# Performance work log

Measured on AMD Instinct MI355X. Metric: run time of the kernel, lower is better.

The kernel has to match this reference:

```python
import jax, jax.numpy as jnp
import numpy as np

INF = 1000000000000.0
B, H, EMB = 64, 512, 512
V = 32000
S_ENC, S_SEQ = 512, 512
ENC2 = 512  # 2 * encoder_hidden_dim
NUM_OOV = 50


def setup_inputs() -> dict:
    key = jax.random.key(0)
    ks = jax.random.split(key, 24)
    s = 0.02
    nrm = lambda k, shp: jax.random.normal(k, shp, jnp.float32) * s
    inp = {}
    inp["input_ids"] = jax.random.randint(ks[0], (B,), 0, V)
    inp["prev_context"] = jax.random.normal(ks[1], (B, H), jnp.float32)
    inp["h0"] = jax.random.normal(ks[2], (1, B, H), jnp.float32)
    inp["c0"] = jax.random.normal(ks[3], (1, B, H), jnp.float32)
    inp["encoder_outputs"] = jax.random.normal(ks[4], (B, S_ENC, H), jnp.float32)
    inp["seqs_encoding"] = jax.random.normal(ks[5], (B, S_SEQ, ENC2), jnp.float32)
    inp["seqs_encoding_mask"] = jax.random.randint(ks[6], (B, S_SEQ), 0, 2).astype(bool)
    ext = jax.random.randint(ks[7], (B, S_SEQ), 0, V + NUM_OOV)
    inp["ext_idx"] = ext.at[0, 0].set(V + NUM_OOV - 1)  # pin max so num_oov=NUM_OOV
    # parameters (torch Linear convention: y = x @ W.T + b)
    inp["embed"] = nrm(ks[8], (V, EMB))
    inp["W_reduce"] = nrm(ks[9], (EMB, EMB + H)); inp["b_reduce"] = jnp.zeros((EMB,), jnp.float32)
    inp["W_key"] = nrm(ks[10], (H, H)); inp["b_key"] = jnp.zeros((H,), jnp.float32)
    inp["W_comb"] = nrm(ks[11], (H, 2 * H)); inp["b_comb"] = jnp.zeros((H,), jnp.float32)
    inp["W_seqkey"] = nrm(ks[12], (H, ENC2))
    inp["W_ih"] = nrm(ks[13], (4 * H, EMB)); inp["W_hh"] = nrm(ks[14], (4 * H, H))
    inp["b_ih"] = jnp.zeros((4 * H,), jnp.float32); inp["b_hh"] = jnp.zeros((4 * H,), jnp.float32)
    inp["W_out"] = nrm(ks[15], (V, H)); inp["b_out"] = jnp.zeros((V,), jnp.float32)
    return inp


def reference(input_ids, prev_context, h0, c0, encoder_outputs, seqs_encoding,
              seqs_encoding_mask, ext_idx, embed, W_reduce, b_reduce, W_key, b_key,
              W_comb, b_comb, W_seqkey, W_ih, W_hh, b_ih, b_hh, W_out, b_out):
    # embed + (dropout is identity at p=0 / eval) + reduce
    embedded = embed[input_ids]                                   # [B, EMB]
    x = jnp.concatenate([embedded, prev_context], axis=1) @ W_reduce.T + b_reduce  # [B, EMB]
    # single-step, single-layer LSTM (PyTorch gate order i, f, g, o)
    h, c = h0[0], c0[0]
    gates = x @ W_ih.T + b_ih + h @ W_hh.T + b_hh                 # [B, 4H]
    i, f, g, o = jnp.split(gates, 4, axis=-1)
    c1 = jax.nn.sigmoid(f) * c + jax.nn.sigmoid(i) * jnp.tanh(g)
    h1 = jax.nn.sigmoid(o) * jnp.tanh(c1)                         # [B, H]
    output = h1
    # masked attention over encoder_outputs
    enc_mask = encoder_outputs.sum(axis=-1) == 0                  # [B, S_enc]
    keys = encoder_outputs @ W_key.T + b_key                      # [B, S_enc, H]
    energies = jnp.einsum('bsh,bh->bs', keys, output)
    energies = jnp.where(enc_mask, 1e-12, energies)
    attn_weights = jax.nn.softmax(energies, axis=-1)
    context = jnp.einsum('bs,bsh->bh', attn_weights, encoder_outputs)  # [B, H]
    combined = jnp.tanh(jnp.concatenate([output, context], axis=1) @ W_comb.T + b_comb)
    logits = combined @ W_out.T + b_out                           # [B, V]
    # masked attention energies over token sequence for the copy mechanism
    seq_keys = jnp.tanh(seqs_encoding @ W_seqkey.T)               # [B, S_seq, H]
    seq_energies = jnp.einsum('bsh,bh->bs', seq_keys, output)
    seq_energies = jnp.where(seqs_encoding_mask, 1e-12, seq_energies)
    # extended vocab + scatter_max pointer-copy
    extended = jnp.concatenate([logits, jnp.zeros((B, NUM_OOV), logits.dtype)], axis=1)  # [B, V+OOV]
    copy = jnp.full_like(extended, -INF)
    copy = copy.at[jnp.arange(B)[:, None], ext_idx].max(seq_energies)
    copy = jnp.where(copy == -INF, 0.0, copy)
    out = extended + copy
    out = jnp.where(out == 0.0, -INF, out)
    out = jax.nn.log_softmax(out, axis=1)
    return (out, context, h1[None], c1[None], attn_weights)
```

## Files before the change

### kernel.cpp

```cpp
#include <hip/hip_runtime.h>
#include <math.h>

#define B_N    64
#define H_N    512
#define V_N    32000
#define S_N    512
#define VEXT   32050
#define INF_F  1000000000000.0f

typedef __attribute__((ext_vector_type(4))) float floatx4;
typedef __attribute__((ext_vector_type(8))) __bf16 bf16x8;

#define OFF_OUT0 0
#define OFF_CTX  (B_N * VEXT)
#define OFF_H1   (OFF_CTX + B_N * H_N)
#define OFF_C1   (OFF_H1 + B_N * H_N)
#define OFF_ATTN (OFF_C1 + B_N * H_N)

#define WS_FLAG   0
#define WS_X      16
#define WS_GATES  (WS_X + B_N * H_N)
#define WS_Q      (WS_GATES + B_N * 4 * H_N)
#define WS_KB     (WS_Q + B_N * H_N)
#define WS_EN     (WS_KB + B_N)
#define WS_COMB   (WS_EN + B_N * S_N)
#define WS_SEQE   (WS_COMB + B_N * H_N)
#define WS_WSKBF  (WS_SEQE + B_N * S_N)
#define WS_LOGITS (WS_WSKBF + (H_N * H_N) / 2)
#define WS_COPY   (WS_LOGITS + B_N * V_N)
#define WS_RMAX   (WS_COPY + B_N * VEXT)
#define WS_RSUM   (WS_RMAX + B_N)

__device__ __forceinline__ float sigm(float x) { return 1.0f / (1.0f + expf(-x)); }

__device__ __forceinline__ unsigned short f2bf(float f) {
    unsigned u = __float_as_uint(f);
    u += 0x7fffu + ((u >> 16) & 1u);
    return (unsigned short)(u >> 16);
}

__device__ __forceinline__ unsigned enc_f(float f) {
    unsigned u = __float_as_uint(f);
    return (u & 0x80000000u) ? ~u : (u | 0x80000000u);
}
__device__ __forceinline__ float dec_f(unsigned e) {
    unsigned u = (e & 0x80000000u) ? (e & 0x7fffffffu) : ~e;
    return __uint_as_float(u);
}

__global__ void kDetect(const unsigned int* __restrict__ m, int* __restrict__ flag) {
    __shared__ int any;
    if (threadIdx.x == 0) any = 0;
    __syncthreads();
    int loc = 0;
    for (int i = threadIdx.x; i < 8192; i += 256) loc |= (m[i] > 1u) ? 1 : 0;
    if (loc) any = 1;
    __syncthreads();
    if (threadIdx.x == 0) *flag = any;
}

__global__ void kConvertW(const float* __restrict__ W, unsigned short* __restrict__ wsk) {
    const int i = (blockIdx.x * 256 + threadIdx.x) * 4;
    float4 v = *(const float4*)(W + i);
    ushort4 h;
    h.x = f2bf(v.x); h.y = f2bf(v.y); h.z = f2bf(v.z); h.w = f2bf(v.w);
    *(ushort4*)(wsk + i) = h;
}

__global__ void kFillCopy(unsigned int* __restrict__ copyenc,
                          unsigned int* __restrict__ rmax, float* __restrict__ rsum) {
    const unsigned NE = enc_f(-INF_F);
    if (blockIdx.x == 0 && threadIdx.x < B_N) {
        rmax[threadIdx.x] = 0u;
        rsum[threadIdx.x] = 0.0f;
    }
    int i0 = (blockIdx.x * 256 + threadIdx.x) * 4;
#pragma unroll
    for (int k = 0; k < 4; k++) {
        int i = i0 + k;
        if (i < B_N * VEXT) copyenc[i] = NE;
    }
}

__global__ __launch_bounds__(256) void kEmbedReduce(
        const int* __restrict__ ids, const float* __restrict__ embed,
        const float* __restrict__ pctx, const float* __restrict__ Wred,
        const float* __restrict__ bred, float* __restrict__ x) {
    __shared__ float xc[1024];
    const int tid = threadIdx.x;
    const int b = blockIdx.x >> 1, half = blockIdx.x & 1;
    const float* er = embed + (size_t)ids[b] * 512;
    xc[tid] = er[tid];               xc[tid + 256] = er[tid + 256];
    xc[512 + tid] = pctx[b * 512 + tid]; xc[512 + tid + 256] = pctx[b * 512 + tid + 256];
    __syncthreads();
    const int j = half * 256 + tid;
    const float4* w4 = (const float4*)(Wred + (size_t)j * 1024);
    const float4* x4 = (const float4*)xc;
    float acc = bred[j];
    for (int k = 0; k < 256; k++) {
        float4 w = w4[k], xv = x4[k];
        acc += w.x * xv.x + w.y * xv.y + w.z * xv.z + w.w * xv.w;
    }
    x[b * 512 + j] = acc;
}

__global__ __launch_bounds__(256) void kGates(
        const float* __restrict__ x, const float* __restrict__ h0,
        const float* __restrict__ Wih, const float* __restrict__ Whh,
        const float* __restrict__ bih, const float* __restrict__ bhh,
        float* __restrict__ gates) {
    __shared__ float xl[512], hl[512];
    const int tid = threadIdx.x;
    const int b = blockIdx.x >> 3, part = blockIdx.x & 7;
    xl[tid] = x[b * 512 + tid];  xl[tid + 256] = x[b * 512 + tid + 256];
    hl[tid] = h0[b * 512 + tid]; hl[tid + 256] = h0[b * 512 + tid + 256];
    __syncthreads();
    const int j = part * 256 + tid;
    const float4* wi4 = (const float4*)(Wih + (size_t)j * 512);
    const float4* wh4 = (const float4*)(Whh + (size_t)j * 512);
    const float4* x4 = (const float4*)xl;
    const float4* h4 = (const float4*)hl;
    float acc = bih[j] + bhh[j];
    for (int k = 0; k < 128; k++) {
        float4 w = wi4[k], xv = x4[k];
        acc += w.x * xv.x + w.y * xv.y + w.z * xv.z + w.w * xv.w;
    }
    for (int k = 0; k < 128; k++) {
        float4 w = wh4[k], hv = h4[k];
        acc += w.x * hv.x + w.y * hv.y + w.z * hv.z + w.w * hv.w;
    }
    gates[(size_t)b * 2048 + j] = acc;
}

__global__ __launch_bounds__(256) void kLstm(
        const float* __restrict__ gates, const float* __restrict__ c0,
        float* __restrict__ h1o, float* __restrict__ c1o) {
    const int idx = blockIdx.x * 256 + threadIdx.x;
    const int b = idx >> 9, j = idx & 511;
    const float gi = gates[(size_t)b * 2048 + j];
    const float gf = gates[(size_t)b * 2048 + 512 + j];
    const float gg = gates[(size_t)b * 2048 + 1024 + j];
    const float go = gates[(size_t)b * 2048 + 1536 + j];
    const float cp = c0[idx];
    const float c1 = sigm(gf) * cp + sigm(gi) * tanhf(gg);
    const float h1 = sigm(go) * tanhf(c1);
    h1o[idx] = h1;
    c1o[idx] = c1;
}

__global__ __launch_bounds__(256) void kQ(
        const float* __restrict__ h1, const float* __restrict__ Wkey,
        const float* __restrict__ bkey, float* __restrict__ q, float* __restrict__ kb) {
    __shared__ float hl[512];
    __shared__ float rd[256];
    const int tid = threadIdx.x;
    const int b = blockIdx.x >> 1, half = blockIdx.x & 1;
    hl[tid] = h1[b * 512 + tid]; hl[tid + 256] = h1[b * 512 + tid + 256];
    __syncthreads();
    const int k = half * 256 + tid;
    float acc = 0.f;
#pragma unroll 4
    for (int h = 0; h < 512; h++) acc += hl[h] * Wkey[(size_t)h * 512 + k];
    q[b * 512 + k] = acc;
    if (half == 0) {
        float p = bkey[tid] * hl[tid] + bkey[tid + 256] * hl[tid + 256];
        rd[tid] = p; __syncthreads();
        for (int st = 128; st > 0; st >>= 1) {
            if (tid < st) rd[tid] += rd[tid + st];
            __syncthreads();
        }
        if (tid == 0) kb[b] = rd[0];
    }
}

__global__ __launch_bounds__(256) void kEnergies(
        const float* __restrict__ enc, const float* __restrict__ q,
        const float* __restrict__ kb, float* __restrict__ energ) {
    __shared__ float ql[512];
    __shared__ float pe[256], ps[256];
    const int tid = threadIdx.x;
    const int b = blockIdx.x >> 2;
    const int sc = (blockIdx.x & 3) * 128;
    ql[tid] = q[b * 512 + tid]; ql[tid + 256] = q[b * 512 + tid + 256];
    __syncthreads();
    const int r = tid & 127, hi = tid >> 7;
    const float4* row4 = (const float4*)(enc + (size_t)(b * 512 + sc + r) * 512 + hi * 256);
    const float4* q4 = (const float4*)(ql + hi * 256);
    float e = 0.f, ssum = 0.f;
#pragma unroll 4
    for (int k = 0; k < 64; k++) {
        float4 ev = row4[k], qv = q4[k];
        e += ev.x * qv.x + ev.y * qv.y + ev.z * qv.z + ev.w * qv.w;
        ssum += ev.x + ev.y + ev.z + ev.w;
    }
    pe[tid] = e; ps[tid] = ssum;
    __syncthreads();
    if (tid < 128) {
        float ee = pe[tid] + pe[tid + 128] + kb[b];
        float sm = ps[tid] + ps[tid + 128];
        if (sm == 0.0f) ee = 1e-12f;
        energ[b * 512 + sc + tid] = ee;
    }
}

__global__ __launch_bounds__(256) void kSoftmax(
        const float* __restrict__ energ, float* __restrict__ attn) {
    __shared__ float el[512];
    __shared__ float rd[256];
    const int tid = threadIdx.x, b = blockIdx.x;
    el[tid] = energ[b * 512 + tid]; el[tid + 256] = energ[b * 512 + tid + 256];
    __syncthreads();
    rd[tid] = fmaxf(el[tid], el[tid + 256]); __syncthreads();
    for (int st = 128; st > 0; st >>= 1) {
        if (tid < st) rd[tid] = fmaxf(rd[tid], rd[tid + st]);
        __syncthreads();
    }
    const float m = rd[0]; __syncthreads();
    float v0 = expf(el[tid] - m), v1 = expf(el[tid + 256] - m);
    rd[tid] = v0 + v1; __syncthreads();
    for (int st = 128; st > 0; st >>= 1) {
        if (tid < st) rd[tid] += rd[tid + st];
        __syncthreads();
    }
    const float inv = 1.0f / rd[0];
    attn[b * 512 + tid] = v0 * inv;
    attn[b * 512 + tid + 256] = v1 * inv;
}

__global__ __launch_bounds__(256) void kContext(
        const float* __restrict__ enc, const float* __restrict__ attn,
        float* __restrict__ ctx) {
    __shared__ float al[64];
    const int tid = threadIdx.x;
    const int b = blockIdx.x >> 3, sc = (blockIdx.x & 7) * 64;
    if (tid < 64) al[tid] = attn[b * 512 + sc + tid];
    __syncthreads();
    float a0 = 0.f, a1 = 0.f;
    for (int s = 0; s < 64; s++) {
        const float* row = enc + (size_t)(b * 512 + sc + s) * 512;
        const float av = al[s];
        a0 += av * row[tid];
        a1 += av * row[tid + 256];
    }
    atomicAdd(&ctx[b * 512 + tid], a0);
    atomicAdd(&ctx[b * 512 + tid + 256], a1);
}

__global__ __launch_bounds__(256) void kCombined(
        const float* __restrict__ h1, const float* __restrict__ ctx,
        const float* __restrict__ Wcomb, const float* __restrict__ bcomb,
        float* __restrict__ comb) {
    __shared__ float hc[1024];
    const int tid = threadIdx.x;
    const int b = blockIdx.x >> 1, half = blockIdx.x & 1;
    hc[tid] = h1[b * 512 + tid];        hc[tid + 256] = h1[b * 512 + tid + 256];
    hc[512 + tid] = ctx[b * 512 + tid]; hc[512 + tid + 256] = ctx[b * 512 + tid + 256];
    __syncthreads();
    const int j = half * 256 + tid;
    const float4* w4 = (const float4*)(Wcomb + (size_t)j * 1024);
    const float4* x4 = (const float4*)hc;
    float acc = bcomb[j];
    for (int k = 0; k < 256; k++) {
        float4 w = w4[k], xv = x4[k];
        acc += w.x * xv.x + w.y * xv.y + w.z * xv.z + w.w * xv.w;
    }
    comb[b * 512 + j] = tanhf(acc);
}

__global__ __launch_bounds__(256) void kLogits(
        const float* __restrict__ comb, const float* __restrict__ Wout,
        const float* __restrict__ bout, float* __restrict__ logits) {
    __shared__ float cl[4][32][64];
    const int tid = threadIdx.x;
    const int vt = tid & 63, kq = tid >> 6;
    const int v = blockIdx.x * 64 + vt;
    float acc[64];
#pragma unroll
    for (int i = 0; i < 64; i++) acc[i] = 0.f;
    for (int kc = 0; kc < 4; kc++) {
        __syncthreads();
        {
            const float4* s4 = (const float4*)(comb + (size_t)vt * 512 + kq * 128 + kc * 32);
#pragma unroll
            for (int qq = 0; qq < 8; qq++) {
                float4 vv = s4[qq];
                cl[kq][qq * 4 + 0][vt] = vv.x; cl[kq][qq * 4 + 1][vt] = vv.y;
                cl[kq][qq * 4 + 2][vt] = vv.z; cl[kq][qq * 4 + 3][vt] = vv.w;
            }
        }
        __syncthreads();
        float wreg[32];
        const float4* w4 = (const float4*)(Wout + (size_t)v * 512 + kq * 128 + kc * 32);
#pragma unroll
        for (int qq = 0; qq < 8; qq++) {
            float4 wv = w4[qq];
            wreg[qq * 4 + 0] = wv.x; wreg[qq * 4 + 1] = wv.y;
            wreg[qq * 4 + 2] = wv.z; wreg[qq * 4 + 3] = wv.w;
        }
#pragma unroll
        for (int kk = 0; kk < 32; kk++) {
            const float wv = wreg[kk];
            const float4* cp = (const float4*)&cl[kq][kk][0];
#pragma unroll
            for (int b4 = 0; b4 < 16; b4++) {
                float4 c4 = cp[b4];
                acc[b4 * 4 + 0] += wv * c4.x; acc[b4 * 4 + 1] += wv * c4.y;
                acc[b4 * 4 + 2] += wv * c4.z; acc[b4 * 4 + 3] += wv * c4.w;
            }
        }
    }
    float* red = &cl[0][0][0];
    __syncthreads();
    if (kq >= 2) {
#pragma unroll
        for (int b = 0; b < 64; b++) red[(kq - 2) * 4096 + vt * 64 + b] = acc[b];
    }
    __syncthreads();
    if (kq < 2) {
#pragma unroll
        for (int b = 0; b < 64; b++) acc[b] += red[kq * 4096 + vt * 64 + b];
    }
    __syncthreads();
    if (kq == 1) {
#pragma unroll
        for (int b = 0; b < 64; b++) red[vt * 64 + b] = acc[b];
    }
    __syncthreads();
    if (kq == 0) {
        const float bo = bout[v];
#pragma unroll
        for (int b = 0; b < 64; b++)
            logits[(size_t)b * 32000 + v] = acc[b] + red[vt * 64 + b] + bo;
    }
}

__global__ __launch_bounds__(512) void kSeqGemm(
        const float* __restrict__ seqs, const unsigned short* __restrict__ wsk,
        const float* __restrict__ h1g, float* __restrict__ seq_e) {
    __shared__ unsigned short a_lds[64 * 40];
    __shared__ unsigned short b_lds[512 * 40];
    __shared__ float h1l[512];
    __shared__ float partf[8][64];
    const int tid = threadIdx.x;
    const int m0 = blockIdx.x * 64;
    const int b = m0 >> 9;
    const int w = tid >> 6;
    const int lane = tid & 63;
    const int quad = lane >> 4;
    const int c16 = lane & 15;

    h1l[tid] = h1g[b * 512 + tid];

    floatx4 acc[4][4];
    const floatx4 zf = {0.f, 0.f, 0.f, 0.f};
#pragma unroll
    for (int i = 0; i < 4; i++)
#pragma unroll
        for (int j = 0; j < 4; j++) acc[i][j] = zf;

    const int arow = tid >> 3, aseg = tid & 7;
    for (int kc = 0; kc < 16; kc++) {
        const int k0 = kc * 32;
        __syncthreads();
        {
            const float4 v = *(const float4*)(seqs + (size_t)(m0 + arow) * 512 + k0 + aseg * 4);
            ushort4 hv;
            hv.x = f2bf(v.x); hv.y = f2bf(v.y); hv.z = f2bf(v.z); hv.w = f2bf(v.w);
            *(ushort4*)&a_lds[arow * 40 + aseg * 4] = hv;
        }
        {
            const uint4* sp = (const uint4*)(wsk + (size_t)tid * 512 + k0);
            uint4* dp = (uint4*)&b_lds[tid * 40];
            dp[0] = sp[0]; dp[1] = sp[1]; dp[2] = sp[2]; dp[3] = sp[3];
        }
        __syncthreads();
        bf16x8 af[4], bfr[4];
#pragma unroll
        for (int ms = 0; ms < 4; ms++)
            af[ms] = *(const bf16x8*)&a_lds[(ms * 16 + c16) * 40 + quad * 8];
#pragma unroll
        for (int nt = 0; nt < 4; nt++)
            bfr[nt] = *(const bf16x8*)&b_lds[(w * 64 + nt * 16 + c16) * 40 + quad * 8];
#pragma unroll
        for (int ms = 0; ms < 4; ms++)
#pragma unroll
            for (int nt = 0; nt < 4; nt++)
                acc[ms][nt] = __builtin_amdgcn_mfma_f32_16x16x32_bf16(
                    af[ms], bfr[nt], acc[ms][nt], 0, 0, 0);
    }
    float psum[16];
#pragma unroll
    for (int i = 0; i < 16; i++) psum[i] = 0.f;
#pragma unroll
    for (int ms = 0; ms < 4; ms++)
#pragma unroll
        for (int nt = 0; nt < 4; nt++) {
            const float hv = h1l[w * 64 + nt * 16 + c16];
#pragma unroll
            for (int r = 0; r < 4; r++)
                psum[ms * 4 + r] += tanhf(acc[ms][nt][r]) * hv;
        }
#pragma unroll
    for (int d = 1; d < 16; d <<= 1)
#pragma unroll
        for (int i = 0; i < 16; i++) psum[i] += __shfl_xor(psum[i], d);
    if (c16 == 0) {
#pragma unroll
        for (int ms = 0; ms < 4; ms++)
#pragma unroll
            for (int r = 0; r < 4; r++)
                partf[w][ms * 16 + quad * 4 + r] = psum[ms * 4 + r];
    }
    __syncthreads();
    if (tid < 64) {
        float s = 0.f;
#pragma unroll
        for (int ww = 0; ww < 8; ww++) s += partf[ww][tid];
        seq_e[m0 + tid] = s;
    }
}

__global__ __launch_bounds__(512) void kScatter(
        const float* __restrict__ seq_e, const void* __restrict__ mask,
        const int* __restrict__ extix, const int* __restrict__ flag,
        unsigned int* __restrict__ copyenc) {
    const int tid = threadIdx.x, b = blockIdx.x;
    float e = seq_e[b * 512 + tid];
    bool mk;
    if (*flag) mk = ((const unsigned char*)mask)[b * 512 + tid] != 0;
    else       mk = ((const int*)mask)[b * 512 + tid] != 0;
    if (mk) e = 1e-12f;
    const int idx = extix[b * 512 + tid];
    atomicMax(&copyenc[(size_t)b * VEXT + idx], enc_f(e));
}

__global__ __launch_bounds__(256) void kFinal1(
        const float* __restrict__ logits, const unsigned int* __restrict__ copyenc,
        float* __restrict__ out0, unsigned int* __restrict__ rmax) {
    __shared__ float rd[4];
    const int tid = threadIdx.x;
    const int b = blockIdx.x >> 4, chunk = blockIdx.x & 15;
    const int base = chunk * 2048 + tid;
    const float* lrow = logits + (size_t)b * 32000;
    const unsigned int* crow = copyenc + (size_t)b * VEXT;
    float* orow = out0 + (size_t)b * VEXT;
    float lm = -3.0e38f;
#pragma unroll
    for (int k = 0; k < 8; k++) {
        const int j = base + k * 256;
        if (j < VEXT) {
            float ext = (j < 32000) ? lrow[j] : 0.0f;
            float cv = dec_f(crow[j]);
            if (cv == -INF_F) cv = 0.0f;
            float o = ext + cv;
            if (o == 0.0f) o = -INF_F;
            orow[j] = o;
            lm = fmaxf(lm, o);
        }
    }
#pragma unroll
    for (int d = 1; d < 64; d <<= 1) lm = fmaxf(lm, __shfl_xor(lm, d));
    if ((tid & 63) == 0) rd[tid >> 6] = lm;
    __syncthreads();
    if (tid == 0) {
        float m = fmaxf(fmaxf(rd[0], rd[1]), fmaxf(rd[2], rd[3]));
        atomicMax(&rmax[b], enc_f(m));
    }
}

__global__ __launch_bounds__(256) void kFinal2(
        const float* __restrict__ out0, const unsigned int* __restrict__ rmax,
        float* __restrict__ rsum) {
    __shared__ float rd[4];
    const int tid = threadIdx.x;
    const int b = blockIdx.x >> 4, chunk = blockIdx.x & 15;
    const int base = chunk * 2048 + tid;
    const float* orow = out0 + (size_t)b * VEXT;
    const float m = dec_f(rmax[b]);
    float s = 0.f;
#pragma unroll
    for (int k = 0; k < 8; k++) {
        const int j = base + k * 256;
        if (j < VEXT) s += expf(orow[j] - m);
    }
#pragma unroll
    for (int d = 1; d < 64; d <<= 1) s += __shfl_xor(s, d);
    if ((tid & 63) == 0) rd[tid >> 6] = s;
    __syncthreads();
    if (tid == 0) atomicAdd(&rsum[b], rd[0] + rd[1] + rd[2] + rd[3]);
}

__global__ __launch_bounds__(256) void kFinal3(
        float* __restrict__ out0, const unsigned int* __restrict__ rmax,
        const float* __restrict__ rsum) {
    const int tid = threadIdx.x;
    const int b = blockIdx.x >> 4, chunk = blockIdx.x & 15;
    const int base = chunk * 2048 + tid;
    float* orow = out0 + (size_t)b * VEXT;
    const float lse = dec_f(rmax[b]) + logf(rsum[b]);
#pragma unroll
    for (int k = 0; k < 8; k++) {
        const int j = base + k * 256;
        if (j < VEXT) orow[j] -= lse;
    }
}

extern "C" void kernel_launch(void* const* d_in, const int* in_sizes, int n_in,
                              void* d_out, int out_size, void* d_ws, size_t ws_size,
                              hipStream_t stream) {
    const int*   ids   = (const int*)d_in[0];
    const float* pctx  = (const float*)d_in[1];
    const float* h0    = (const float*)d_in[2];
    const float* c0    = (const float*)d_in[3];
    const float* enc   = (const float*)d_in[4];
    const float* seqs  = (const float*)d_in[5];
    const void*  mask  = d_in[6];
    const int*   extix = (const int*)d_in[7];
    const float* embed = (const float*)d_in[8];
    const float* Wred  = (const float*)d_in[9];
    const float* bred  = (const float*)d_in[10];
    const float* Wkey  = (const float*)d_in[11];
    const float* bkey  = (const float*)d_in[12];
    const float* Wcomb = (const float*)d_in[13];
    const float* bcomb = (const float*)d_in[14];
    const float* Wseqk = (const float*)d_in[15];
    const float* Wih   = (const float*)d_in[16];
    const float* Whh   = (const float*)d_in[17];
    const float* bih   = (const float*)d_in[18];
    const float* bhh   = (const float*)d_in[19];
    const float* Wout  = (const float*)d_in[20];
    const float* bout  = (const float*)d_in[21];
    (void)in_sizes; (void)n_in; (void)out_size; (void)ws_size;

    float* out = (float*)d_out;
    float* ws = (float*)d_ws;
    int* flag = (int*)ws;
    float* xws = ws + WS_X;
    float* gatesws = ws + WS_GATES;
    float* qws = ws + WS_Q;
    float* kbws = ws + WS_KB;
    float* enws = ws + WS_EN;
    float* combws = ws + WS_COMB;
    float* seqews = ws + WS_SEQE;
    unsigned short* wsk = (unsigned short*)(ws + WS_WSKBF);
    float* logitsws = ws + WS_LOGITS;
    unsigned int* copyenc = (unsigned int*)(ws + WS_COPY);
    unsigned int* rmax = (unsigned int*)(ws + WS_RMAX);
    float* rsum = ws + WS_RSUM;

    kDetect<<<1, 256, 0, stream>>>((const unsigned int*)mask, flag);
    kConvertW<<<256, 256, 0, stream>>>(Wseqk, wsk);
    kFillCopy<<<2004, 256, 0, stream>>>(copyenc, rmax, rsum);
    kEmbedReduce<<<128, 256, 0, stream>>>(ids, embed, pctx, Wred, bred, xws);
    kGates<<<512, 256, 0, stream>>>(xws, h0, Wih, Whh, bih, bhh, gatesws);
    kLstm<<<128, 256, 0, stream>>>(gatesws, c0, out + OFF_H1, out + OFF_C1);
    kQ<<<128, 256, 0, stream>>>(out + OFF_H1, Wkey, bkey, qws, kbws);
    kEnergies<<<256, 256, 0, stream>>>(enc, qws, kbws, enws);
    kSoftmax<<<64, 256, 0, stream>>>(enws, out + OFF_ATTN);
    hipMemsetAsync(out + OFF_CTX, 0, (size_t)B_N * H_N * sizeof(float), stream);
    kContext<<<512, 256, 0, stream>>>(enc, out + OFF_ATTN, out + OFF_CTX);
    kCombined<<<128, 256, 0, stream>>>(out + OFF_H1, out + OFF_CTX, Wcomb, bcomb, combws);
    kLogits<<<500, 256, 0, stream>>>(combws, Wout, bout, logitsws);
    kSeqGemm<<<512, 512, 0, stream>>>(seqs, wsk, out + OFF_H1, seqews);
    kScatter<<<64, 512, 0, stream>>>(seqews, mask, extix, flag, copyenc);
    kFinal1<<<1024, 256, 0, stream>>>(logitsws, copyenc, out + OFF_OUT0, rmax);
    kFinal2<<<1024, 256, 0, stream>>>(out + OFF_OUT0, rmax, rsum);
    kFinal3<<<1024, 256, 0, stream>>>(out + OFF_OUT0, rmax, rsum);
}
```

Baseline: 607.2 us.

## Pre-swizzle seq-key weights into MFMA fragment order and stage full A tile once

The bf16 conversion kernel now writes W_seqkey in a layout where each lane's 8-element MFMA B fragment is contiguous, so kSeqGemm reads B fragments straight from global memory instead of staging them through LDS every k-step. The A tile (64 rows x 512 K) is converted to bf16 and loaded into LDS once up front, which removes the per-iteration double __syncthreads. This trades LDS traffic and barriers for direct global/L2 fragment loads and a larger LDS footprint (about 66KB), which may limit occupancy despite the launch-bounds hint.

```diff
diff --git a/kernel.cpp b/kernel.cpp
--- a/kernel.cpp
+++ b/kernel.cpp
@@ -59,12 +59,18 @@
     if (threadIdx.x == 0) *flag = any;
 }
 
-__global__ void kConvertW(const float* __restrict__ W, unsigned short* __restrict__ wsk) {
-    const int i = (blockIdx.x * 256 + threadIdx.x) * 4;
-    float4 v = *(const float4*)(W + i);
-    ushort4 h;
-    h.x = f2bf(v.x); h.y = f2bf(v.y); h.z = f2bf(v.z); h.w = f2bf(v.w);
-    *(ushort4*)(wsk + i) = h;
+__global__ void kConvertW(const float* __restrict__ W, unsigned short* __restrict__ swz) {
+    const int g = blockIdx.x * 256 + threadIdx.x;
+    const int t = g >> 10, kc = (g >> 6) & 15, lane = g & 63;
+    const int r = t * 16 + (lane & 15);
+    const int k = kc * 32 + (lane >> 4) * 8;
+    const float4 v0 = *(const float4*)(W + (size_t)r * 512 + k);
+    const float4 v1 = *(const float4*)(W + (size_t)r * 512 + k + 4);
+    ushort4 h0, h1;
+    h0.x = f2bf(v0.x); h0.y = f2bf(v0.y); h0.z = f2bf(v0.z); h0.w = f2bf(v0.w);
+    h1.x = f2bf(v1.x); h1.y = f2bf(v1.y); h1.z = f2bf(v1.z); h1.w = f2bf(v1.w);
+    *(ushort4*)(swz + (size_t)g * 8) = h0;
+    *(ushort4*)(swz + (size_t)g * 8 + 4) = h1;
 }
 
 __global__ void kFillCopy(unsigned int* __restrict__ copyenc,
@@ -334,11 +340,11 @@
     }
 }
 
-__global__ __launch_bounds__(512) void kSeqGemm(
-        const float* __restrict__ seqs, const unsigned short* __restrict__ wsk,
+#define A_STRIDE 520
+__global__ __launch_bounds__(512, 4) void kSeqGemm(
+        const float* __restrict__ seqs, const unsigned short* __restrict__ swz,
         const float* __restrict__ h1g, float* __restrict__ seq_e) {
-    __shared__ unsigned short a_lds[64 * 40];
-    __shared__ unsigned short b_lds[512 * 40];
+    __shared__ unsigned short a_lds[64 * A_STRIDE];
     __shared__ float h1l[512];
     __shared__ float partf[8][64];
     const int tid = threadIdx.x;
@@ -351,6 +357,20 @@
 
     h1l[tid] = h1g[b * 512 + tid];
 
+    {
+        const int row = tid >> 3, seg = tid & 7;
+        const float* src = seqs + (size_t)(m0 + row) * 512 + seg * 4;
+        unsigned short* dst = &a_lds[row * A_STRIDE + seg * 4];
+#pragma unroll
+        for (int i = 0; i < 16; i++) {
+            float4 v = *(const float4*)(src + i * 32);
+            ushort4 hv;
+            hv.x = f2bf(v.x); hv.y = f2bf(v.y); hv.z = f2bf(v.z); hv.w = f2bf(v.w);
+            *(ushort4*)(dst + i * 32) = hv;
+        }
+    }
+    __syncthreads();
+
     floatx4 acc[4][4];
     const floatx4 zf = {0.f, 0.f, 0.f, 0.f};
 #pragma unroll
@@ -358,29 +378,16 @@
 #pragma unroll
         for (int j = 0; j < 4; j++) acc[i][j] = zf;
 
-    const int arow = tid >> 3, aseg = tid & 7;
+    const unsigned short* bbase = swz + (size_t)((w * 4) * 16) * 512 + (size_t)lane * 8;
+#pragma unroll 2
     for (int kc = 0; kc < 16; kc++) {
-        const int k0 = kc * 32;
-        __syncthreads();
-        {
-            const float4 v = *(const float4*)(seqs + (size_t)(m0 + arow) * 512 + k0 + aseg * 4);
-            ushort4 hv;
-            hv.x = f2bf(v.x); hv.y = f2bf(v.y); hv.z = f2bf(v.z); hv.w = f2bf(v.w);
-            *(ushort4*)&a_lds[arow * 40 + aseg * 4] = hv;
-        }
-        {
-            const uint4* sp = (const uint4*)(wsk + (size_t)tid * 512 + k0);
-            uint4* dp = (uint4*)&b_lds[tid * 40];
-            dp[0] = sp[0]; dp[1] = sp[1]; dp[2] = sp[2]; dp[3] = sp[3];
-        }
-        __syncthreads();
         bf16x8 af[4], bfr[4];
 #pragma unroll
+        for (int nt = 0; nt < 4; nt++)
+            bfr[nt] = *(const bf16x8*)(bbase + (size_t)(nt * 16 + kc) * 512);
+#pragma unroll
         for (int ms = 0; ms < 4; ms++)
-            af[ms] = *(const bf16x8*)&a_lds[(ms * 16 + c16) * 40 + quad * 8];
-#pragma unroll
-        for (int nt = 0; nt < 4; nt++)
-            bfr[nt] = *(const bf16x8*)&b_lds[(w * 64 + nt * 16 + c16) * 40 + quad * 8];
+            af[ms] = *(const bf16x8*)&a_lds[(ms * 16 + c16) * A_STRIDE + kc * 32 + quad * 8];
 #pragma unroll
         for (int ms = 0; ms < 4; ms++)
 #pragma unroll
@@ -388,6 +395,7 @@
                 acc[ms][nt] = __builtin_amdgcn_mfma_f32_16x16x32_bf16(
                     af[ms], bfr[nt], acc[ms][nt], 0, 0, 0);
     }
+
     float psum[16];
 #pragma unroll
     for (int i = 0; i < 16; i++) psum[i] = 0.f;
@@ -549,7 +557,7 @@
     float* rsum = ws + WS_RSUM;
 
     kDetect<<<1, 256, 0, stream>>>((const unsigned int*)mask, flag);
-    kConvertW<<<256, 256, 0, stream>>>(Wseqk, wsk);
+    kConvertW<<<128, 256, 0, stream>>>(Wseqk, wsk);
     kFillCopy<<<2004, 256, 0, stream>>>(copyenc, rmax, rsum);
     kEmbedReduce<<<128, 256, 0, stream>>>(ids, embed, pctx, Wred, bred, xws);
     kGates<<<512, 256, 0, stream>>>(xws, h0, Wih, Whh, bih, bhh, gatesws);
```

Result: faster. 571.7 us (-5.9%).
